# Performance work log

Hardware: AMD Instinct MI355X
Metric: run time of the kernel (lower is better)

## Reference

```python
import jax, jax.numpy as jnp
import numpy as np

E = 768          # embed_dim
H = 12           # n_attention_heads
D = E // H       # head_embed_dim = 64
S = 197          # seq_len (196 patches + CLS)
MRD = 13         # max_relative_dist
GRID = 14        # sqrt(S - 1)
B = 64
NUM_EMB = 2 * MRD + 1 + 1  # embedding table rows (index 0 reserved for CLS)


def _relative_distances(pos):
    # pos: (S-1,) int. distances clamped, shifted to [1, 2*MRD+1], padded with 0 for CLS.
    d = pos[None, :] - pos[:, None]
    d = np.clip(d, -MRD, MRD) + MRD + 1
    d = np.pad(d, ((1, 0), (1, 0)), constant_values=0)
    return jnp.asarray(d, dtype=jnp.int32)  # (S, S)


def setup_inputs() -> dict:
    key = jax.random.key(0)
    ks = jax.random.split(key, 16)
    s_lin = 1.0 / np.sqrt(E)
    inp = {
        "x": jax.random.normal(ks[0], (B, S, E), jnp.float32),
        "Wq": jax.random.normal(ks[1], (E, E), jnp.float32) * s_lin,
        "bq": jnp.zeros((E,), jnp.float32),
        "Wk": jax.random.normal(ks[2], (E, E), jnp.float32) * s_lin,
        "bk": jnp.zeros((E,), jnp.float32),
        "Wv": jax.random.normal(ks[3], (E, E), jnp.float32) * s_lin,
        "bv": jnp.zeros((E,), jnp.float32),
        "Wo": jax.random.normal(ks[4], (E, E), jnp.float32) * s_lin,
        "bo": jnp.zeros((E,), jnp.float32),
        "q_tab_x": jax.random.normal(ks[5], (NUM_EMB, D // 2), jnp.float32),
        "q_tab_y": jax.random.normal(ks[6], (NUM_EMB, D // 2), jnp.float32),
        "v_tab_x": jax.random.normal(ks[7], (NUM_EMB, D // 2), jnp.float32),
        "v_tab_y": jax.random.normal(ks[8], (NUM_EMB, D // 2), jnp.float32),
    }
    p = np.arange(S - 1)
    inp["x_dist"] = _relative_distances(p % GRID)   # (S, S) int32
    inp["y_dist"] = _relative_distances(p // GRID)  # (S, S) int32
    return inp


def reference(x, Wq, bq, Wk, bk, Wv, bv, Wo, bo,
              q_tab_x, q_tab_y, v_tab_x, v_tab_y, x_dist, y_dist):
    b, s, e = x.shape
    # QKV projections -> (b, h, s, d)
    xq = (x @ Wq.T + bq).reshape(b, s, H, D).transpose(0, 2, 1, 3)
    xk = (x @ Wk.T + bk).reshape(b, s, H, D).transpose(0, 2, 1, 3)
    xv = (x @ Wv.T + bv).reshape(b, s, H, D).transpose(0, 2, 1, 3)

    # content logits
    attn = jnp.einsum('bhqd,bhkd->bhqk', xq, xk)

    # query relative-position logits: pos embedding (q, k, d) gathered from x/y tables
    q_pos = jnp.concatenate([q_tab_x[x_dist], q_tab_y[y_dist]], axis=-1)  # (s, s, d)
    attn = attn + jnp.einsum('bhqd,qkd->bhqk', xq, q_pos)

    attn = jax.nn.softmax(attn / np.float32(np.sqrt(D)), axis=-1)

    out = jnp.einsum('bhqk,bhkd->bhqd', attn, xv)

    # value relative-position contribution
    v_pos = jnp.concatenate([v_tab_x[x_dist], v_tab_y[y_dist]], axis=-1)  # (s, s, d)
    out = out + jnp.einsum('bhqk,qkd->bhqd', attn, v_pos)

    out = out.transpose(0, 2, 1, 3).reshape(b, s, e)
    return out @ Wo.T + bo
```

## Files before the change

kernel.cpp:

```cpp
#include <hip/hip_runtime.h>
#include <math.h>

#define SEQ 197
#define EMB 768
#define NH  12
#define HD  64
#define NE  28
#define SK  208
#define VP  232
#define PP  232
#define EP  232
#define HP  66
#define TP  66
#define NW  7
#define NT  448

typedef __attribute__((ext_vector_type(8))) __bf16 bf16x8;
typedef __attribute__((ext_vector_type(4))) float  f32x4;

__device__ __forceinline__ unsigned short f2bf(float f) {
    unsigned u = __float_as_uint(f);
    u += 0x7fffu + ((u >> 16) & 1u);
    return (unsigned short)(u >> 16);
}
__device__ __forceinline__ float bfl(unsigned u) { return __uint_as_float(u << 16); }

__device__ __forceinline__ void gl_lds16(const ushort* g, ushort* l) {
    __builtin_amdgcn_global_load_lds(
        (const __attribute__((address_space(1))) unsigned int*)g,
        (__attribute__((address_space(3))) unsigned int*)l, 16, 0, 0);
}

__global__ void cvt_k(const float* __restrict__ src, ushort* __restrict__ dst, int n4) {
    int i = blockIdx.x * 256 + threadIdx.x;
    if (i < n4) {
        float4 v = ((const float4*)src)[i];
        ushort4 o = { f2bf(v.x), f2bf(v.y), f2bf(v.z), f2bf(v.w) };
        ((ushort4*)dst)[i] = o;
    }
}

__global__ void cvt_w4(const float* __restrict__ wq, const float* __restrict__ wk,
                       const float* __restrict__ wv, const float* __restrict__ wo,
                       ushort* __restrict__ wqkv, ushort* __restrict__ wob) {
    int i = blockIdx.x * 256 + threadIdx.x;
    if (i >= 4 * 147456) return;
    int seg = i / 147456, r = i - seg * 147456;
    const float* s = (seg == 0) ? wq : (seg == 1) ? wk : (seg == 2) ? wv : wo;
    float4 v = ((const float4*)s)[r];
    ushort4 o = { f2bf(v.x), f2bf(v.y), f2bf(v.z), f2bf(v.w) };
    if (seg < 3) ((ushort4*)wqkv)[(size_t)seg * 147456 + r] = o;
    else         ((ushort4*)wob)[r] = o;
}

__global__ __launch_bounds__(256) void rxy_gemm(
    const ushort* __restrict__ xq,
    const float* __restrict__ qtx, const float* __restrict__ qty,
    ushort* __restrict__ r_o)
{
    __shared__ __align__(16) ushort qtab_s[64][66];

    const int bh = blockIdx.x;
    const size_t base = (size_t)bh * SEQ * HD;
    const int tid = threadIdx.x;
    const int w = tid >> 6, lane = tid & 63;
    const int g = lane >> 4, c15 = lane & 15;

    for (int idx = tid; idx < 64 * 64; idx += 256) {
        const int e = idx >> 6, d = idx & 63;
        float v = 0.f;
        if (e < 28)      { if (d < 32)  v = qtx[e * 32 + d]; }
        else if (e < 56) { if (d >= 32) v = qty[(e - 28) * 32 + (d - 32)]; }
        qtab_s[e][d] = f2bf(v);
    }
    __syncthreads();

    for (int qt = w; qt < 13; qt += 4) {
        const int qrow = qt * 16 + c15;
        const int qld = (qrow < SEQ) ? qrow : SEQ - 1;
        const bf16x8 qa0 = *(const bf16x8*)(xq + base + (size_t)qld * HD + g * 8);
        const bf16x8 qa1 = *(const bf16x8*)(xq + base + (size_t)qld * HD + 32 + g * 8);
#pragma unroll
        for (int et = 0; et < 4; et++) {
            bf16x8 t0 = *(const bf16x8*)&qtab_s[et * 16 + c15][g * 8];
            bf16x8 t1 = *(const bf16x8*)&qtab_s[et * 16 + c15][32 + g * 8];
            f32x4 a = (f32x4)0.f;
            a = __builtin_amdgcn_mfma_f32_16x16x32_bf16(qa0, t0, a, 0, 0, 0);
            a = __builtin_amdgcn_mfma_f32_16x16x32_bf16(qa1, t1, a, 0, 0, 0);
#pragma unroll
            for (int r = 0; r < 4; r++) {
                const int q = qt * 16 + g * 4 + r;
                const int e = et * 16 + c15;
                if (q < SEQ && e < 56)
                    r_o[((size_t)bh * SEQ + q) * 56 + e] = f2bf(a[r]);
            }
        }
    }
}

template<int MODE>
__global__ __launch_bounds__(256, 2) void gemm_k64(
    const ushort* __restrict__ A, const ushort* __restrict__ W,
    const float* __restrict__ b0, const float* __restrict__ b1, const float* __restrict__ b2,
    ushort* __restrict__ q_o, ushort* __restrict__ k_o, ushort* __restrict__ v_o,
    float* __restrict__ f_o, int M)
{
    __shared__ __align__(16) ushort As[128 * 64];
    __shared__ __align__(16) ushort Bs[128 * 64];

    const int tid  = threadIdx.x;
    const int w    = tid >> 6, lane = tid & 63;
    const int wr   = w >> 1,  wc   = w & 1;

    const int nmt = gridDim.x, nnt = gridDim.y;
    const int lin = blockIdx.y * nmt + blockIdx.x;
    const int gsz = 8 * nnt;
    const int grp = lin / gsz;
    const int rr  = lin - grp * gsz;
    int mig = nmt - grp * 8; if (mig > 8) mig = 8;
    const int mt  = grp * 8 + rr % mig;
    const int nt  = rr / mig;
    const int m0  = mt * 128;
    const int n0  = nt * 128;

    int arow[4], asrc[4];
#pragma unroll
    for (int i = 0; i < 4; i++) {
        const int gidx = tid + i * 256;
        const int row = gidx >> 3, ch = gidx & 7;
        arow[i] = row;
        asrc[i] = (ch ^ (row & 7)) * 8;
    }

    f32x4 acc[4][4];
#pragma unroll
    for (int m = 0; m < 4; m++)
#pragma unroll
        for (int n = 0; n < 4; n++) acc[m][n] = (f32x4)0.f;

    for (int k0 = 0; k0 < EMB; k0 += 64) {
#pragma unroll
        for (int i = 0; i < 4; i++) {
            int ra = m0 + arow[i]; if (ra >= M) ra = M - 1;
            gl_lds16(A + (size_t)ra * EMB + k0 + asrc[i], As + (tid + i * 256) * 8);
            gl_lds16(W + (size_t)(n0 + arow[i]) * EMB + k0 + asrc[i], Bs + (tid + i * 256) * 8);
        }
        __syncthreads();

#pragma unroll
        for (int kk = 0; kk < 2; kk++) {
            bf16x8 af[4], bfr[4];
#pragma unroll
            for (int m = 0; m < 4; m++) {
                const int row = wr * 64 + m * 16 + (lane & 15);
                af[m] = *(const bf16x8*)&As[row * 64 + (((kk * 4 + (lane >> 4)) ^ (row & 7)) << 3)];
            }
#pragma unroll
            for (int n = 0; n < 4; n++) {
                const int row = wc * 64 + n * 16 + (lane & 15);
                bfr[n] = *(const bf16x8*)&Bs[row * 64 + (((kk * 4 + (lane >> 4)) ^ (row & 7)) << 3)];
            }
#pragma unroll
            for (int m = 0; m < 4; m++)
#pragma unroll
                for (int n = 0; n < 4; n++)
                    acc[m][n] = __builtin_amdgcn_mfma_f32_16x16x32_bf16(af[m], bfr[n], acc[m][n], 0, 0, 0);
        }
        __syncthreads();
    }

    const int mat = n0 / EMB;
    const int nr  = n0 - mat * EMB;
    const float* bias = (mat == 0) ? b0 : (mat == 1) ? b1 : b2;
    ushort* dst = (mat == 0) ? q_o : (mat == 1) ? k_o : v_o;

#pragma unroll
    for (int m = 0; m < 4; m++) {
#pragma unroll
        for (int r = 0; r < 4; r++) {
            const int gm = m0 + wr * 64 + m * 16 + (lane >> 4) * 4 + r;
            if (gm >= M) continue;
            const int bb = gm / SEQ, ss = gm - bb * SEQ;
#pragma unroll
            for (int n = 0; n < 4; n++) {
                const int col = nr + wc * 64 + n * 16 + (lane & 15);
                if (MODE == 0) {
                    const float v = acc[m][n][r] + bias[col];
                    dst[(((size_t)bb * NH + (col >> 6)) * SEQ + ss) * HD + (col & 63)] = f2bf(v);
                } else {
                    f_o[(size_t)gm * EMB + col] = acc[m][n][r] + b0[col];
                }
            }
        }
    }
}

__global__ __launch_bounds__(NT) void attn_mfma(
    const ushort* __restrict__ xq, const ushort* __restrict__ xk, const ushort* __restrict__ xv,
    const ushort* __restrict__ rxy_g,
    const float* __restrict__ v_tab_x, const float* __restrict__ v_tab_y,
    const int* __restrict__ x_dist, const int* __restrict__ y_dist,
    ushort* __restrict__ ao)
{
    __shared__ __align__(16) ushort K_s[SK * HD];
    __shared__ __align__(16) ushort EXYs_s[SK * 40];
    __shared__ __align__(16) ushort EXYT_s[32 * EP];
    __shared__ __align__(16) ushort VT_s[HD * VP];
    __shared__ __align__(16) ushort P_s[NW * 16 * PP];
    __shared__ __align__(16) ushort vt_s[HD * TP];
    __shared__ __align__(16) ushort h_s[NW][16][HP];
    __shared__ ushort cxy_s[SEQ];

    const int bh = blockIdx.x;
    const int b  = bh / NH;
    const int h  = bh % NH;
    const size_t base = (size_t)bh * SEQ * HD;
    const ushort* __restrict__ rxy_b = rxy_g + (size_t)bh * SEQ * 56;
    const int tid = threadIdx.x;
    const int w = tid >> 6, lane = tid & 63;
    const int g = lane >> 4, c15 = lane & 15;

    for (int idx = tid; idx < SK * 8; idx += NT) {
        const int r = idx >> 3, c = idx & 7;
        uint4 v = make_uint4(0, 0, 0, 0);
        if (r < SEQ) v = *(const uint4*)(xk + base + r * HD + c * 8);
        *(uint4*)&K_s[r * HD + ((c ^ (r & 7)) << 3)] = v;
    }
    for (int idx = tid; idx < SK * 40 / 8; idx += NT)
        *(uint4*)&EXYs_s[idx * 8] = make_uint4(0, 0, 0, 0);
    for (int idx = tid; idx < 32 * EP / 8; idx += NT)
        *(uint4*)&EXYT_s[idx * 8] = make_uint4(0, 0, 0, 0);
    for (int idx = tid; idx < HD * (VP - SEQ); idx += NT) {
        const int d = idx / (VP - SEQ), k = SEQ + idx - d * (VP - SEQ);
        VT_s[d * VP + k] = 0;
    }
    for (int idx = tid; idx < NW * 16 * 3; idx += NT) {
        const int row = idx / 3, c = idx - row * 3;
        *(uint4*)&P_s[row * PP + 208 + c * 8] = make_uint4(0, 0, 0, 0);
    }
    for (int k = tid; k < SEQ; k += NT)
        cxy_s[k] = (ushort)((x_dist[SEQ + k] & 0xff) | ((y_dist[SEQ + k] & 0xff) << 8));
    for (int idx = tid; idx < 16 * 8 * 13; idx += NT) {
        const int kq = idx & 15, t = idx >> 4;
        const int db = t & 7, kh = t >> 3;
        const int k = kh * 16 + kq;
        if (k >= SEQ) continue;
        uint4 v = *(const uint4*)(xv + base + k * HD + db * 8);
        ushort* col = &VT_s[(db * 8) * VP + k];
        col[0 * VP] = (ushort)(v.x); col[1 * VP] = (ushort)(v.x >> 16);
        col[2 * VP] = (ushort)(v.y); col[3 * VP] = (ushort)(v.y >> 16);
        col[4 * VP] = (ushort)(v.z); col[5 * VP] = (ushort)(v.z >> 16);
        col[6 * VP] = (ushort)(v.w); col[7 * VP] = (ushort)(v.w >> 16);
    }
    for (int idx = tid; idx < HD * 64; idx += NT) {
        const int d = idx >> 6, e = idx & 63;
        float v = 0.f;
        if (d < 32) { if (e < 28) v = v_tab_x[e * 32 + d]; }
        else        { if (e >= 28 && e < 56) v = v_tab_y[(e - 28) * 32 + (d - 32)]; }
        vt_s[d * TP + e] = f2bf(v);
    }
    __syncthreads();
    for (int k = tid; k < SEQ; k += NT) {
        const int cx = (k == 0) ? 14 : ((cxy_s[k] & 0xff) - 14);
        const int cy = (k == 0) ? 14 : ((cxy_s[k] >> 8) - 14);
        const ushort one = 0x3f80;
        EXYs_s[k * 40 + cx]        = one;
        EXYs_s[k * 40 + 16 + cy]   = one;
        EXYT_s[cx * EP + k]        = one;
        EXYT_s[(16 + cy) * EP + k] = one;
    }
    __syncthreads();

    for (int qt = w; qt < 13; qt += NW) {
        const int qrow = qt * 16 + c15;
        const int qld  = (qrow < SEQ) ? qrow : (SEQ - 1);
        const bf16x8 qa0 = *(const bf16x8*)(xq + base + (size_t)qld * HD + g * 8);
        const bf16x8 qa1 = *(const bf16x8*)(xq + base + (size_t)qld * HD + 32 + g * 8);

        uint4 up;
        {
            const ushort* rrow = rxy_b + qld * 56;
            const int cxq = (qld > 0) ? ((cxy_s[qld] & 0xff) - 14) : 0;
            const int cyq = (qld > 0) ? ((cxy_s[qld] >> 8) - 14) : 0;
            unsigned uu[4] = {0, 0, 0, 0};
#pragma unroll
            for (int j = 0; j < 8; j++) {
                const int c = g * 8 + j;
                ushort v;
                if (qld == 0)      v = (c == 15 || c == 31) ? (ushort)0 : rrow[(c < 16) ? 0 : 28];
                else if (c < 14)   v = rrow[c - cxq + 14];
                else if (c == 14)  v = rrow[0];
                else if (c == 15)  v = 0;
                else if (c < 30)   v = rrow[28 + (c - 16) - cyq + 14];
                else if (c == 30)  v = rrow[28];
                else               v = 0;
                uu[j >> 1] |= ((unsigned)v) << ((j & 1) * 16);
            }
            up.x = uu[0]; up.y = uu[1]; up.z = uu[2]; up.w = uu[3];
        }
        const bf16x8 qa2 = *(bf16x8*)&up;

        {
            uint4* hz = (uint4*)h_s[w];
            for (int i = lane; i < 16 * HP / 8; i += 64) hz[i] = make_uint4(0, 0, 0, 0);
        }

        const int q4 = qt * 16 + 4 * g;
        float sum[4] = {0.f, 0.f, 0.f, 0.f};

#pragma unroll
        for (int kt = 0; kt < 13; kt++) {
            const int kr = kt * 16 + c15;
            bf16x8 kf0 = *(const bf16x8*)&K_s[kr * HD + (((0 + g) ^ (kr & 7)) << 3)];
            bf16x8 kf1 = *(const bf16x8*)&K_s[kr * HD + (((4 + g) ^ (kr & 7)) << 3)];
            bf16x8 kf2 = *(const bf16x8*)&EXYs_s[kr * 40 + g * 8];
            f32x4 a = (f32x4)0.f;
            a = __builtin_amdgcn_mfma_f32_16x16x32_bf16(qa0, kf0, a, 0, 0, 0);
            a = __builtin_amdgcn_mfma_f32_16x16x32_bf16(qa1, kf1, a, 0, 0, 0);
            a = __builtin_amdgcn_mfma_f32_16x16x32_bf16(qa2, kf2, a, 0, 0, 0);
#pragma unroll
            for (int r = 0; r < 4; r++) {
                const float l = a[r] * 0.125f - 8.0f;
                const float p = (kr < SEQ) ? __expf(l) : 0.f;
                sum[r] += p;
                P_s[(w * 16 + 4 * g + r) * PP + kr] = f2bf(p);
            }
        }
        float inv[4];
#pragma unroll
        for (int r = 0; r < 4; r++) {
            sum[r] += __shfl_xor(sum[r], 1);
            sum[r] += __shfl_xor(sum[r], 2);
            sum[r] += __shfl_xor(sum[r], 4);
            sum[r] += __shfl_xor(sum[r], 8);
            inv[r] = 1.f / sum[r];
        }

        f32x4 px0 = (f32x4)0.f, px1 = (f32x4)0.f;
#pragma unroll
        for (int ks = 0; ks < 7; ks++) {
            bf16x8 pf = *(const bf16x8*)&P_s[(w * 16 + c15) * PP + ks * 32 + g * 8];
            bf16x8 e0 = *(const bf16x8*)&EXYT_s[c15 * EP + ks * 32 + g * 8];
            bf16x8 e1 = *(const bf16x8*)&EXYT_s[(16 + c15) * EP + ks * 32 + g * 8];
            px0 = __builtin_amdgcn_mfma_f32_16x16x32_bf16(pf, e0, px0, 0, 0, 0);
            px1 = __builtin_amdgcn_mfma_f32_16x16x32_bf16(pf, e1, px1, 0, 0, 0);
        }

        float sx = px0[0], sy = px1[0];
        if (qt == 0) {
            sx += __shfl_xor(sx, 1); sx += __shfl_xor(sx, 2);
            sx += __shfl_xor(sx, 4); sx += __shfl_xor(sx, 8);
            sy += __shfl_xor(sy, 1); sy += __shfl_xor(sy, 2);
            sy += __shfl_xor(sy, 4); sy += __shfl_xor(sy, 8);
        }

#pragma unroll
        for (int r = 0; r < 4; r++) {
            const int q = q4 + r;
            if (q >= SEQ) continue;
            const int ql = 4 * g + r;
            if (q == 0) {
                if (c15 == 14) { h_s[w][ql][0] = f2bf(sx); h_s[w][ql][28] = f2bf(sy); }
            } else {
                const int cxq2 = (cxy_s[q] & 0xff) - 14;
                const int cyq2 = (cxy_s[q] >> 8) - 14;
                if (c15 < 14) {
                    h_s[w][ql][c15 - cxq2 + 14]      = f2bf(px0[r]);
                    h_s[w][ql][28 + c15 - cyq2 + 14] = f2bf(px1[r]);
                } else if (c15 == 14) {
                    h_s[w][ql][0]  = f2bf(px0[r]);
                    h_s[w][ql][28] = f2bf(px1[r]);
                }
            }
        }

        f32x4 o[4];
#pragma unroll
        for (int dt = 0; dt < 4; dt++) o[dt] = (f32x4)0.f;
#pragma unroll
        for (int ks = 0; ks < 7; ks++) {
            bf16x8 pf = *(const bf16x8*)&P_s[(w * 16 + c15) * PP + ks * 32 + g * 8];
#pragma unroll
            for (int dt = 0; dt < 4; dt++) {
                bf16x8 vf = *(const bf16x8*)&VT_s[(dt * 16 + c15) * VP + ks * 32 + g * 8];
                o[dt] = __builtin_amdgcn_mfma_f32_16x16x32_bf16(pf, vf, o[dt], 0, 0, 0);
            }
        }
#pragma unroll
        for (int ks2 = 0; ks2 < 2; ks2++) {
            bf16x8 hf = *(const bf16x8*)&h_s[w][c15][ks2 * 32 + g * 8];
#pragma unroll
            for (int dt = 0; dt < 4; dt++) {
                bf16x8 tf = *(const bf16x8*)&vt_s[(dt * 16 + c15) * TP + ks2 * 32 + g * 8];
                o[dt] = __builtin_amdgcn_mfma_f32_16x16x32_bf16(hf, tf, o[dt], 0, 0, 0);
            }
        }

#pragma unroll
        for (int dt = 0; dt < 4; dt++) {
            const int d = dt * 16 + c15;
#pragma unroll
            for (int r = 0; r < 4; r++) {
                const int q = q4 + r;
                if (q < SEQ)
                    ao[((size_t)(b * SEQ + q)) * EMB + h * HD + d] = f2bf(o[dt][r] * inv[r]);
            }
        }
    }
}

extern "C" void kernel_launch(void* const* d_in, const int* in_sizes, int n_in,
                              void* d_out, int out_size, void* d_ws, size_t ws_size,
                              hipStream_t stream) {
    const float* x       = (const float*)d_in[0];
    const float* Wq      = (const float*)d_in[1];
    const float* bq      = (const float*)d_in[2];
    const float* Wk      = (const float*)d_in[3];
    const float* bk      = (const float*)d_in[4];
    const float* Wv      = (const float*)d_in[5];
    const float* bv      = (const float*)d_in[6];
    const float* Wo      = (const float*)d_in[7];
    const float* bo      = (const float*)d_in[8];
    const float* q_tab_x = (const float*)d_in[9];
    const float* q_tab_y = (const float*)d_in[10];
    const float* v_tab_x = (const float*)d_in[11];
    const float* v_tab_y = (const float*)d_in[12];
    const int*   x_dist  = (const int*)d_in[13];
    const int*   y_dist  = (const int*)d_in[14];
    float* out = (float*)d_out;

    const int M  = in_sizes[0] / EMB;
    const int Bc = M / SEQ;

    ushort* xb   = (ushort*)d_ws;
    ushort* wqkv = xb   + (size_t)M * EMB;
    ushort* wob  = wqkv + (size_t)2304 * EMB;
    ushort* xqb  = wob  + (size_t)EMB * EMB;
    ushort* xkb  = xqb  + (size_t)M * EMB;
    ushort* xvb  = xkb  + (size_t)M * EMB;
    ushort* aob  = xvb  + (size_t)M * EMB;
    ushort* r_o  = aob  + (size_t)M * EMB;

    const int n4x = M * EMB / 4;
    cvt_k<<<dim3((n4x + 255) / 256), dim3(256), 0, stream>>>(x, xb, n4x);
    cvt_w4<<<dim3(2304), dim3(256), 0, stream>>>(Wq, Wk, Wv, Wo, wqkv, wob);

    gemm_k64<0><<<dim3((M + 127) / 128, 18), dim3(256), 0, stream>>>(
        xb, wqkv, bq, bk, bv, xqb, xkb, xvb, nullptr, M);

    rxy_gemm<<<dim3(Bc * NH), dim3(256), 0, stream>>>(xqb, q_tab_x, q_tab_y, r_o);

    attn_mfma<<<dim3(Bc * NH), dim3(NT), 0, stream>>>(
        xqb, xkb, xvb, r_o, v_tab_x, v_tab_y, x_dist, y_dist, aob);

    gemm_k64<1><<<dim3((M + 127) / 128, 6), dim3(256), 0, stream>>>(
        aob, wob, bo, nullptr, nullptr, nullptr, nullptr, nullptr, out, M);
}
```

Before: 158.9 us.

## Merge conversion kernels, batch rxy heads per block, prefetch next Q tile

Fuses the x and weight bf16 conversion kernels into one launch. rxy_gemm now processes four batch-heads per block, so the q-table setup is amortised and fewer blocks launch. In attn_mfma, each wave loads the Q fragments and relative-position row for its second q-tile before processing the first, and the softmax sum reduction moves later to overlap with MFMA work. These cut launch and setup overhead and hide load latency, at the cost of extra registers and less block parallelism in rxy_gemm.

```diff
diff --git a/kernel.cpp b/kernel.cpp
--- a/kernel.cpp
+++ b/kernel.cpp
@@ -31,21 +31,21 @@
         (__attribute__((address_space(3))) unsigned int*)l, 16, 0, 0);
 }
 
-__global__ void cvt_k(const float* __restrict__ src, ushort* __restrict__ dst, int n4) {
+__global__ void cvt_all(const float* __restrict__ x,
+                        const float* __restrict__ wq, const float* __restrict__ wk,
+                        const float* __restrict__ wv, const float* __restrict__ wo,
+                        ushort* __restrict__ xb,
+                        ushort* __restrict__ wqkv, ushort* __restrict__ wob, int n4x) {
     int i = blockIdx.x * 256 + threadIdx.x;
-    if (i < n4) {
-        float4 v = ((const float4*)src)[i];
+    if (i < n4x) {
+        float4 v = ((const float4*)x)[i];
         ushort4 o = { f2bf(v.x), f2bf(v.y), f2bf(v.z), f2bf(v.w) };
-        ((ushort4*)dst)[i] = o;
-    }
-}
-
-__global__ void cvt_w4(const float* __restrict__ wq, const float* __restrict__ wk,
-                       const float* __restrict__ wv, const float* __restrict__ wo,
-                       ushort* __restrict__ wqkv, ushort* __restrict__ wob) {
-    int i = blockIdx.x * 256 + threadIdx.x;
-    if (i >= 4 * 147456) return;
-    int seg = i / 147456, r = i - seg * 147456;
+        ((ushort4*)xb)[i] = o;
+        return;
+    }
+    int j = i - n4x;
+    if (j >= 4 * 147456) return;
+    int seg = j / 147456, r = j - seg * 147456;
     const float* s = (seg == 0) ? wq : (seg == 1) ? wk : (seg == 2) ? wv : wo;
     float4 v = ((const float4*)s)[r];
     ushort4 o = { f2bf(v.x), f2bf(v.y), f2bf(v.z), f2bf(v.w) };
@@ -60,8 +60,6 @@
 {
     __shared__ __align__(16) ushort qtab_s[64][66];
 
-    const int bh = blockIdx.x;
-    const size_t base = (size_t)bh * SEQ * HD;
     const int tid = threadIdx.x;
     const int w = tid >> 6, lane = tid & 63;
     const int g = lane >> 4, c15 = lane & 15;
@@ -75,24 +73,28 @@
     }
     __syncthreads();
 
-    for (int qt = w; qt < 13; qt += 4) {
-        const int qrow = qt * 16 + c15;
-        const int qld = (qrow < SEQ) ? qrow : SEQ - 1;
-        const bf16x8 qa0 = *(const bf16x8*)(xq + base + (size_t)qld * HD + g * 8);
-        const bf16x8 qa1 = *(const bf16x8*)(xq + base + (size_t)qld * HD + 32 + g * 8);
-#pragma unroll
-        for (int et = 0; et < 4; et++) {
-            bf16x8 t0 = *(const bf16x8*)&qtab_s[et * 16 + c15][g * 8];
-            bf16x8 t1 = *(const bf16x8*)&qtab_s[et * 16 + c15][32 + g * 8];
-            f32x4 a = (f32x4)0.f;
-            a = __builtin_amdgcn_mfma_f32_16x16x32_bf16(qa0, t0, a, 0, 0, 0);
-            a = __builtin_amdgcn_mfma_f32_16x16x32_bf16(qa1, t1, a, 0, 0, 0);
-#pragma unroll
-            for (int r = 0; r < 4; r++) {
-                const int q = qt * 16 + g * 4 + r;
-                const int e = et * 16 + c15;
-                if (q < SEQ && e < 56)
-                    r_o[((size_t)bh * SEQ + q) * 56 + e] = f2bf(a[r]);
+    for (int u = 0; u < 4; u++) {
+        const int bh = blockIdx.x * 4 + u;
+        const size_t base = (size_t)bh * SEQ * HD;
+        for (int qt = w; qt < 13; qt += 4) {
+            const int qrow = qt * 16 + c15;
+            const int qld = (qrow < SEQ) ? qrow : SEQ - 1;
+            const bf16x8 qa0 = *(const bf16x8*)(xq + base + (size_t)qld * HD + g * 8);
+            const bf16x8 qa1 = *(const bf16x8*)(xq + base + (size_t)qld * HD + 32 + g * 8);
+#pragma unroll
+            for (int et = 0; et < 4; et++) {
+                bf16x8 t0 = *(const bf16x8*)&qtab_s[et * 16 + c15][g * 8];
+                bf16x8 t1 = *(const bf16x8*)&qtab_s[et * 16 + c15][32 + g * 8];
+                f32x4 a = (f32x4)0.f;
+                a = __builtin_amdgcn_mfma_f32_16x16x32_bf16(qa0, t0, a, 0, 0, 0);
+                a = __builtin_amdgcn_mfma_f32_16x16x32_bf16(qa1, t1, a, 0, 0, 0);
+#pragma unroll
+                for (int r = 0; r < 4; r++) {
+                    const int q = qt * 16 + g * 4 + r;
+                    const int e = et * 16 + c15;
+                    if (q < SEQ && e < 56)
+                        r_o[((size_t)bh * SEQ + q) * 56 + e] = f2bf(a[r]);
+                }
             }
         }
     }
@@ -271,33 +273,43 @@
     }
     __syncthreads();
 
-    for (int qt = w; qt < 13; qt += NW) {
+    auto LOADQ = [&](int qt, bf16x8& qa0, bf16x8& qa1, uint4& up) {
         const int qrow = qt * 16 + c15;
         const int qld  = (qrow < SEQ) ? qrow : (SEQ - 1);
-        const bf16x8 qa0 = *(const bf16x8*)(xq + base + (size_t)qld * HD + g * 8);
-        const bf16x8 qa1 = *(const bf16x8*)(xq + base + (size_t)qld * HD + 32 + g * 8);
-
-        uint4 up;
-        {
-            const ushort* rrow = rxy_b + qld * 56;
-            const int cxq = (qld > 0) ? ((cxy_s[qld] & 0xff) - 14) : 0;
-            const int cyq = (qld > 0) ? ((cxy_s[qld] >> 8) - 14) : 0;
-            unsigned uu[4] = {0, 0, 0, 0};
-#pragma unroll
-            for (int j = 0; j < 8; j++) {
-                const int c = g * 8 + j;
-                ushort v;
-                if (qld == 0)      v = (c == 15 || c == 31) ? (ushort)0 : rrow[(c < 16) ? 0 : 28];
-                else if (c < 14)   v = rrow[c - cxq + 14];
-                else if (c == 14)  v = rrow[0];
-                else if (c == 15)  v = 0;
-                else if (c < 30)   v = rrow[28 + (c - 16) - cyq + 14];
-                else if (c == 30)  v = rrow[28];
-                else               v = 0;
-                uu[j >> 1] |= ((unsigned)v) << ((j & 1) * 16);
-            }
-            up.x = uu[0]; up.y = uu[1]; up.z = uu[2]; up.w = uu[3];
-        }
+        qa0 = *(const bf16x8*)(xq + base + (size_t)qld * HD + g * 8);
+        qa1 = *(const bf16x8*)(xq + base + (size_t)qld * HD + 32 + g * 8);
+        const ushort* rrow = rxy_b + qld * 56;
+        const int cxq = (qld > 0) ? ((cxy_s[qld] & 0xff) - 14) : 0;
+        const int cyq = (qld > 0) ? ((cxy_s[qld] >> 8) - 14) : 0;
+        unsigned uu[4] = {0, 0, 0, 0};
+#pragma unroll
+        for (int j = 0; j < 8; j++) {
+            const int c = g * 8 + j;
+            ushort v;
+            if (qld == 0)      v = (c == 15 || c == 31) ? (ushort)0 : rrow[(c < 16) ? 0 : 28];
+            else if (c < 14)   v = rrow[c - cxq + 14];
+            else if (c == 14)  v = rrow[0];
+            else if (c == 15)  v = 0;
+            else if (c < 30)   v = rrow[28 + (c - 16) - cyq + 14];
+            else if (c == 30)  v = rrow[28];
+            else               v = 0;
+            uu[j >> 1] |= ((unsigned)v) << ((j & 1) * 16);
+        }
+        up.x = uu[0]; up.y = uu[1]; up.z = uu[2]; up.w = uu[3];
+    };
+
+    const int qtA = w, qtB = w + NW;
+    bf16x8 qa0, qa1; uint4 up;
+    LOADQ(qtA, qa0, qa1, up);
+
+    for (int it = 0; it < 2; ++it) {
+        const int qt = (it == 0) ? qtA : qtB;
+        if (qt >= 13) break;
+
+        bf16x8 nqa0, nqa1; uint4 nup;
+        const bool haveB = (it == 0) && (qtB < 13);
+        if (haveB) LOADQ(qtB, nqa0, nqa1, nup);
+
         const bf16x8 qa2 = *(bf16x8*)&up;
 
         {
@@ -325,15 +337,6 @@
                 sum[r] += p;
                 P_s[(w * 16 + 4 * g + r) * PP + kr] = f2bf(p);
             }
-        }
-        float inv[4];
-#pragma unroll
-        for (int r = 0; r < 4; r++) {
-            sum[r] += __shfl_xor(sum[r], 1);
-            sum[r] += __shfl_xor(sum[r], 2);
-            sum[r] += __shfl_xor(sum[r], 4);
-            sum[r] += __shfl_xor(sum[r], 8);
-            inv[r] = 1.f / sum[r];
         }
 
         f32x4 px0 = (f32x4)0.f, px1 = (f32x4)0.f;
@@ -396,6 +399,16 @@
             }
         }
 
+        float inv[4];
+#pragma unroll
+        for (int r = 0; r < 4; r++) {
+            sum[r] += __shfl_xor(sum[r], 1);
+            sum[r] += __shfl_xor(sum[r], 2);
+            sum[r] += __shfl_xor(sum[r], 4);
+            sum[r] += __shfl_xor(sum[r], 8);
+            inv[r] = 1.f / sum[r];
+        }
+
 #pragma unroll
         for (int dt = 0; dt < 4; dt++) {
             const int d = dt * 16 + c15;
@@ -406,6 +419,8 @@
                     ao[((size_t)(b * SEQ + q)) * EMB + h * HD + d] = f2bf(o[dt][r] * inv[r]);
             }
         }
+
+        qa0 = nqa0; qa1 = nqa1; up = nup;
     }
 }
 
@@ -442,13 +457,14 @@
     ushort* r_o  = aob  + (size_t)M * EMB;
 
     const int n4x = M * EMB / 4;
-    cvt_k<<<dim3((n4x + 255) / 256), dim3(256), 0, stream>>>(x, xb, n4x);
-    cvt_w4<<<dim3(2304), dim3(256), 0, stream>>>(Wq, Wk, Wv, Wo, wqkv, wob);
+    const int ncvt = n4x + 4 * 147456;
+    cvt_all<<<dim3((ncvt + 255) / 256), dim3(256), 0, stream>>>(
+        x, Wq, Wk, Wv, Wo, xb, wqkv, wob, n4x);
 
     gemm_k64<0><<<dim3((M + 127) / 128, 18), dim3(256), 0, stream>>>(
         xb, wqkv, bq, bk, bv, xqb, xkb, xvb, nullptr, M);
 
-    rxy_gemm<<<dim3(Bc * NH), dim3(256), 0, stream>>>(xqb, q_tab_x, q_tab_y, r_o);
+    rxy_gemm<<<dim3(Bc * NH / 4), dim3(256), 0, stream>>>(xqb, q_tab_x, q_tab_y, r_o);
 
     attn_mfma<<<dim3(Bc * NH), dim3(NT), 0, stream>>>(
         xqb, xkb, xvb, r_o, v_tab_x, v_tab_y, x_dist, y_dist, aob);
```

Result: slower. 165.8 us (+4.3%).
